# Performance work log

Hardware: AMD Instinct MI355X
Metric: run time of the kernel (lower is better)

The kernel has to match this reference:

```python
import jax, jax.numpy as jnp
import numpy as np

BN_EPS = 1e-3
SLOPE = 0.1
K = 100
CLUSTER_TEMP = 5.0


def setup_inputs() -> dict:
    key = jax.random.key(0)
    ks = jax.random.split(key, 5)
    N, Cin, Cout = 8192, 1, 64
    d = 49 * Cout  # (28/4)^2 * out_channels
    return {
        "x": jax.random.normal(ks[0], (N, Cin, 28, 28), jnp.float32),
        "conv1_w": jax.random.normal(ks[1], (128, Cin, 5, 5), jnp.float32) * 0.05,
        "conv1_b": jnp.zeros((128,), jnp.float32),
        "bn1_gamma": jnp.ones((128,), jnp.float32),
        "bn1_beta": jnp.zeros((128,), jnp.float32),
        "bn1_mean": jnp.zeros((128,), jnp.float32),
        "bn1_var": jnp.ones((128,), jnp.float32),
        "conv2_w": jax.random.normal(ks[2], (Cout, 128, 5, 5), jnp.float32) * 0.02,
        "conv2_b": jnp.zeros((Cout,), jnp.float32),
        "bn2_gamma": jnp.ones((Cout,), jnp.float32),
        "bn2_beta": jnp.zeros((Cout,), jnp.float32),
        "bn2_mean": jnp.zeros((Cout,), jnp.float32),
        "bn2_var": jnp.ones((Cout,), jnp.float32),
        "init_mu": jax.random.uniform(ks[3], (K, d), jnp.float32),
        "num_iter": 10,
    }


def _conv_bn_lrelu(x, w, b, gamma, beta, mean, var):
    # Conv2d(k=5, s=2, p=2) -> BatchNorm (eval/running stats) -> LeakyReLU(0.1)
    h = jax.lax.conv_general_dilated(
        x, w, window_strides=(2, 2), padding=[(2, 2), (2, 2)],
        dimension_numbers=("NCHW", "OIHW", "NCHW"))
    h = h + b[None, :, None, None]
    inv = gamma * jax.lax.rsqrt(var + BN_EPS)
    h = h * inv[None, :, None, None] + (beta - mean * inv)[None, :, None, None]
    return jnp.where(h >= 0, h, SLOPE * h)


def _cluster(data, mu, num_iter):
    # Row L2-normalize (equivalent to diag(1/||row||) @ data)
    data = data / jnp.linalg.norm(data, axis=1, keepdims=True)  # [n, d]
    for _ in range(num_iter):
        dist = data @ mu.T                                 # [n, K]
        r = jax.nn.softmax(CLUSTER_TEMP * dist, axis=1)    # [n, K]
        cluster_r = r.sum(axis=0)                          # [K]
        cluster_mean = r.T @ data                          # [K, d]
        mu = cluster_mean / cluster_r[:, None]
    dist = data @ mu.T
    r = jax.nn.softmax(CLUSTER_TEMP * dist, axis=1)
    return mu, r, dist


def reference(x, conv1_w, conv1_b, bn1_gamma, bn1_beta, bn1_mean, bn1_var,
              conv2_w, conv2_b, bn2_gamma, bn2_beta, bn2_mean, bn2_var,
              init_mu, num_iter):
    h = _conv_bn_lrelu(x, conv1_w, conv1_b, bn1_gamma, bn1_beta, bn1_mean, bn1_var)
    h = _conv_bn_lrelu(h, conv2_w, conv2_b, bn2_gamma, bn2_beta, bn2_mean, bn2_var)
    embeds = h.reshape(h.shape[0], -1)                     # [N, 49*Cout]
    mu_init, _, _ = _cluster(embeds, init_mu, int(num_iter))
    mu, r, dist = _cluster(embeds, jax.lax.stop_gradient(mu_init), 1)
    return mu, r, dist
```

## Files before the change

### kernel.cpp

```cpp
#include <hip/hip_runtime.h>
#include <hip/hip_bf16.h>
#include <math.h>

#define BN_EPS 1e-3f
#define SLOPE  0.1f
#define TEMP   5.0f
#define DDIM   3136

typedef __attribute__((ext_vector_type(8))) short bf16x8;
typedef __attribute__((ext_vector_type(4))) float f32x4;

static __device__ __forceinline__ short f2b(float f) {
  __hip_bfloat16 h = __float2bfloat16(f);
  return *reinterpret_cast<short*>(&h);
}

#define W2B_OFF   0u
#define W1B_OFF   102400u
#define DB_OFF    204800u
#define DB_SZ     (8192u*3136u/2u)
#define DT_OFF    (DB_OFF + DB_SZ)
#define DT_SZ     (8192u*3136u/2u)
#define MUB_OFF   (DT_OFF + DT_SZ)
#define MUB_SZ    (112u*3136u/2u)
#define MUF_OFF   (MUB_OFF + MUB_SZ)
#define MUF_SZ    (100u*3136u)
#define CMS_OFF   (MUF_OFF + MUF_SZ)
#define CMS_SZ    (16u*3136u*112u/2u)
#define RT_OFF    (CMS_OFF + CMS_SZ)
#define RT_SZ     (112u*8192u/2u)
#define CR_OFF    (RT_OFF + RT_SZ)

__global__ __launch_bounds__(256) void k_w2b(const float* __restrict__ w2,
                                             __hip_bfloat16* __restrict__ w2b) {
  int idx = blockIdx.x * 256 + threadIdx.x;
  if (idx >= 204800) return;
  int ci   = idx & 31;
  int lr   = (idx >> 5) & 15;
  int rest = idx >> 9;
  int kk   = rest % 100;
  int oct  = rest / 100;
  int oc   = oct * 16 + lr;
  int tap  = kk >> 2;
  int c    = ((kk & 3) << 5) + ci;
  w2b[idx] = __float2bfloat16(w2[(oc * 128 + c) * 25 + tap]);
}

__global__ __launch_bounds__(256) void k_w1b(const float* __restrict__ w1,
                                             __hip_bfloat16* __restrict__ w1b) {
  int idx = blockIdx.x * 256 + threadIdx.x;
  if (idx >= 4096) return;
  int k   = idx & 31;
  int lr  = (idx >> 5) & 15;
  int oct = idx >> 9;
  int oc  = oct * 16 + lr;
  float v = (k < 25) ? w1[oc * 25 + k] : 0.f;
  w1b[idx] = __float2bfloat16(v);
}

__global__ __launch_bounds__(256) void k_conv(
    const float* __restrict__ x,
    const __hip_bfloat16* __restrict__ w1bh, const float* __restrict__ b1,
    const float* __restrict__ g1,  const float* __restrict__ be1,
    const float* __restrict__ mn1, const float* __restrict__ vr1,
    const __hip_bfloat16* __restrict__ w2bh, const float* __restrict__ b2,
    const float* __restrict__ g2,  const float* __restrict__ be2,
    const float* __restrict__ mn2, const float* __restrict__ vr2,
    __hip_bfloat16* __restrict__ db) {
  __shared__ float xs[1024];
  __shared__ float bn2s[128];
  __shared__ float bn1a[128], bn1b[128];
  __shared__ float nrm[4];
  __shared__ __align__(16) __hip_bfloat16 h1s[197 * 128];

  const int t    = threadIdx.x;
  const int img  = blockIdx.x;
  const int lane = t & 63;
  const int wv   = t >> 6;
  const int lr   = lane & 15;
  const int kg   = lane >> 4;
  const short* w2b = (const short*)w2bh;
  const short* w1b = (const short*)w1bh;

  for (int i = t; i < 1024; i += 256) xs[i] = 0.f;
  if (t < 64) {
    float a2 = g2[t] * rsqrtf(vr2[t] + BN_EPS);
    bn2s[t]      = a2;
    bn2s[64 + t] = b2[t] * a2 + be2[t] - mn2[t] * a2;
    ((unsigned*)(h1s + 196 * 128))[t] = 0u;
  }
  if (t < 128) {
    float a1 = g1[t] * rsqrtf(vr1[t] + BN_EPS);
    bn1a[t] = a1;
    bn1b[t] = b1[t] * a1 + be1[t] - mn1[t] * a1;
  }
  __syncthreads();
  const float* xi = x + (size_t)img * 784;
  for (int i = t; i < 784; i += 256) {
    int yy = i / 28, xx = i % 28;
    xs[(yy + 2) * 32 + (xx + 2)] = xi[i];
  }
  __syncthreads();

  {
    bf16x8 a0 = *(const bf16x8*)(w1b + (2 * wv) * 512 + lr * 32 + kg * 8);
    bf16x8 a1 = *(const bf16x8*)(w1b + (2 * wv + 1) * 512 + lr * 32 + kg * 8);
    for (int pt = 0; pt < 13; ++pt) {
      const int px  = pt * 16 + lr;
      const int pxc = (px < 196) ? px : 195;
      const int oy  = pxc / 14, ox = pxc - 14 * (pxc / 14);
      const float* xb = xs + (2 * oy) * 32 + 2 * ox;
      short bs[8];
#pragma unroll
      for (int j = 0; j < 8; ++j) {
        int k   = kg * 8 + j;
        int tap = (k < 25) ? k : 0;
        int kh  = tap / 5, kw = tap - 5 * (tap / 5);
        bs[j] = f2b(xb[kh * 32 + kw]);
      }
      bf16x8 b;
#pragma unroll
      for (int j = 0; j < 8; ++j) b[j] = bs[j];
      f32x4 c0 = {0.f, 0.f, 0.f, 0.f}, c1 = {0.f, 0.f, 0.f, 0.f};
      c0 = __builtin_amdgcn_mfma_f32_16x16x32_bf16(a0, b, c0, 0, 0, 0);
      c1 = __builtin_amdgcn_mfma_f32_16x16x32_bf16(a1, b, c1, 0, 0, 0);
      if (px < 196) {
        const int swz = (px & 7) << 4;
        unsigned w0lo, w0hi, w1lo, w1hi;
        {
          float v[4], u[4];
#pragma unroll
          for (int r = 0; r < 4; ++r) {
            int oc = wv * 32 + kg * 4 + r;
            float h = c0[r] * bn1a[oc] + bn1b[oc];
            v[r] = (h >= 0.f) ? h : SLOPE * h;
            int oc2 = oc + 16;
            float h2 = c1[r] * bn1a[oc2] + bn1b[oc2];
            u[r] = (h2 >= 0.f) ? h2 : SLOPE * h2;
          }
          w0lo = (unsigned)(unsigned short)f2b(v[0]) |
                 ((unsigned)(unsigned short)f2b(v[1]) << 16);
          w0hi = (unsigned)(unsigned short)f2b(v[2]) |
                 ((unsigned)(unsigned short)f2b(v[3]) << 16);
          w1lo = (unsigned)(unsigned short)f2b(u[0]) |
                 ((unsigned)(unsigned short)f2b(u[1]) << 16);
          w1hi = (unsigned)(unsigned short)f2b(u[2]) |
                 ((unsigned)(unsigned short)f2b(u[3]) << 16);
        }
        char* base = (char*)h1s + px * 256;
        const int o0 = ((wv * 32 + kg * 4) * 2) ^ swz;
        const int o1 = ((wv * 32 + 16 + kg * 4) * 2) ^ swz;
        *(uint2*)(base + o0) = make_uint2(w0lo, w0hi);
        *(uint2*)(base + o1) = make_uint2(w1lo, w1hi);
      }
    }
  }
  __syncthreads();

  const int woff  = lr * 32 + kg * 8;
  const int kgoff = kg << 4;
  int pxA[4], oyA[4], oxA[4];
#pragma unroll
  for (int pt = 0; pt < 4; ++pt) {
    int p = pt * 16 + lr;
    pxA[pt] = p;
    oyA[pt] = p / 7;
    oxA[pt] = p - 7 * oyA[pt];
  }

  f32x4 acc[4][4];
#pragma unroll
  for (int oct = 0; oct < 4; ++oct)
#pragma unroll
    for (int pt = 0; pt < 4; ++pt) acc[oct][pt] = (f32x4){0.f, 0.f, 0.f, 0.f};

  const int s0 = 25 * wv, s1e = s0 + 25;
  int curtap = -1;
  int rowB[4], rowS[4];

  auto loadk = [&](int kk, bf16x8* areg, bf16x8* breg) {
    int tap = kk >> 2;
    if (tap != curtap) {
      curtap = tap;
      int kh = tap / 5, kw = tap - 5 * (tap / 5);
#pragma unroll
      for (int pt = 0; pt < 4; ++pt) {
        int iy = 2 * oyA[pt] - 2 + kh;
        int ix = 2 * oxA[pt] - 2 + kw;
        bool val = (pxA[pt] < 49) & ((unsigned)iy < 14u) & ((unsigned)ix < 14u);
        int ip = val ? iy * 14 + ix : 196;
        rowB[pt] = ip * 256;
        rowS[pt] = (ip & 7) << 4;
      }
    }
    int c01 = (kk & 3) << 6;
#pragma unroll
    for (int oct = 0; oct < 4; ++oct)
      areg[oct] = *(const bf16x8*)(w2b + ((oct * 100 + kk) << 9) + woff);
#pragma unroll
    for (int pt = 0; pt < 4; ++pt)
      breg[pt] = *(const bf16x8*)((const char*)h1s + rowB[pt] +
                                  ((c01 | kgoff) ^ rowS[pt]));
  };

  bf16x8 a[4], b[4], an[4], bn_[4];
  loadk(s0, a, b);
  for (int kk = s0; kk < s1e; ++kk) {
    if (kk + 1 < s1e) loadk(kk + 1, an, bn_);
#pragma unroll
    for (int oct = 0; oct < 4; ++oct)
#pragma unroll
      for (int pt = 0; pt < 4; ++pt)
        acc[oct][pt] = __builtin_amdgcn_mfma_f32_16x16x32_bf16(a[oct], b[pt],
                                                               acc[oct][pt], 0, 0, 0);
#pragma unroll
    for (int q = 0; q < 4; ++q) { a[q] = an[q]; b[q] = bn_[q]; }
  }
  __syncthreads();

  float* red = (float*)h1s;
  if (wv != 0) {
#pragma unroll
    for (int oct = 0; oct < 4; ++oct)
#pragma unroll
      for (int pt = 0; pt < 4; ++pt)
#pragma unroll
        for (int r = 0; r < 4; ++r)
          red[(wv - 1) * 4096 + ((oct * 4 + pt) * 4 + r) * 64 + lane] =
              acc[oct][pt][r];
  }
  __syncthreads();
  if (wv == 0) {
#pragma unroll
    for (int oct = 0; oct < 4; ++oct)
#pragma unroll
      for (int pt = 0; pt < 4; ++pt)
#pragma unroll
        for (int r = 0; r < 4; ++r) {
          const int i = (oct * 4 + pt) * 4 + r;
          float v = acc[oct][pt][r] + red[i * 64 + lane] +
                    red[4096 + i * 64 + lane] + red[8192 + i * 64 + lane];
          red[i * 64 + lane] = v;
        }
  }
  __syncthreads();

  float outv[16];
  float ss = 0.f;
#pragma unroll
  for (int pt = 0; pt < 4; ++pt) {
#pragma unroll
    for (int r = 0; r < 4; ++r) {
      const int i = ((wv * 4 + pt) * 4 + r);
      float v = red[i * 64 + lane];
      const int oc = wv * 16 + kg * 4 + r;
      v = v * bn2s[oc] + bn2s[64 + oc];
      v = (v >= 0.f) ? v : SLOPE * v;
      outv[pt * 4 + r] = v;
      if (pxA[pt] < 49) ss += v * v;
    }
  }
#pragma unroll
  for (int m = 1; m < 64; m <<= 1) ss += __shfl_xor(ss, m, 64);
  if (lane == 0) nrm[wv] = ss;
  __syncthreads();
  const float invn = rsqrtf(nrm[0] + nrm[1] + nrm[2] + nrm[3]);
  __hip_bfloat16* dro = db + (size_t)img * DDIM;
#pragma unroll
  for (int pt = 0; pt < 4; ++pt) {
    if (pxA[pt] < 49) {
#pragma unroll
      for (int r = 0; r < 4; ++r) {
        const int oc = wv * 16 + kg * 4 + r;
        dro[oc * 49 + pxA[pt]] = __float2bfloat16(outv[pt * 4 + r] * invn);
      }
    }
  }
}

__global__ __launch_bounds__(256) void k_tr(const __hip_bfloat16* __restrict__ dbh,
                                            __hip_bfloat16* __restrict__ dTh) {
  __shared__ short tile[64][72];
  const int t   = threadIdx.x;
  const int i   = t >> 2;
  const int seg = t & 3;
  const size_t img0 = (size_t)blockIdx.x * 64;
  const size_t d0   = (size_t)blockIdx.y * 64;
  const short* src = (const short*)dbh + (img0 + i) * DDIM + d0 + seg * 16;
  bf16x8 v0 = *(const bf16x8*)src;
  bf16x8 v1 = *(const bf16x8*)(src + 8);
  *(bf16x8*)&tile[i][seg * 16]     = v0;
  *(bf16x8*)&tile[i][seg * 16 + 8] = v1;
  __syncthreads();
  short tmp[16];
#pragma unroll
  for (int k = 0; k < 16; ++k) tmp[k] = tile[seg * 16 + k][i];
  short* dst = (short*)dTh + (d0 + i) * 8192 + img0 + seg * 16;
  *(bf16x8*)dst       = *(bf16x8*)tmp;
  *(bf16x8*)(dst + 8) = *((bf16x8*)tmp + 1);
}

__global__ __launch_bounds__(256) void k_muinit(const float* __restrict__ mu0,
                                                __hip_bfloat16* __restrict__ mub) {
  int idx = blockIdx.x * 256 + threadIdx.x;
  if (idx >= 112 * DDIM) return;
  int j = idx / DDIM, d = idx - j * DDIM;
  float v = (j < 100) ? mu0[j * DDIM + d] : 0.f;
  mub[idx] = __float2bfloat16(v);
}

__global__ __launch_bounds__(512) void k_dsm(
    const __hip_bfloat16* __restrict__ data,
    const __hip_bfloat16* __restrict__ mu,
    __hip_bfloat16* __restrict__ rT,
    float* __restrict__ cr,
    float* __restrict__ outr,
    float* __restrict__ outd,
    int final_flag) {
  __shared__ float red[7][64][29];
  const int t    = threadIdx.x;
  const int lane = t & 63;
  const int wv   = t >> 6;
  const int rowbase = blockIdx.x * 16;
  const int s0 = (98 * wv) >> 3;
  const int s1 = (98 * (wv + 1)) >> 3;
  const int lr = lane & 15;
  const int kg = lane >> 4;

  const __hip_bfloat16* arow = data + (size_t)(rowbase + lr) * DDIM + kg * 8;
  const __hip_bfloat16* brow = mu + (size_t)lr * DDIM + kg * 8;

  f32x4 acc[7];
#pragma unroll
  for (int i = 0; i < 7; ++i) acc[i] = (f32x4){0.f, 0.f, 0.f, 0.f};

  bf16x8 a, b[7], an, bn_[7];
  {
    const int k0 = s0 * 32;
    a = *(const bf16x8*)(arow + k0);
#pragma unroll
    for (int tl = 0; tl < 7; ++tl)
      b[tl] = *(const bf16x8*)(brow + (size_t)tl * 16 * DDIM + k0);
  }
  for (int s = s0; s < s1; ++s) {
    if (s + 1 < s1) {
      const int k1 = (s + 1) * 32;
      an = *(const bf16x8*)(arow + k1);
#pragma unroll
      for (int tl = 0; tl < 7; ++tl)
        bn_[tl] = *(const bf16x8*)(brow + (size_t)tl * 16 * DDIM + k1);
    }
#pragma unroll
    for (int tl = 0; tl < 7; ++tl)
      acc[tl] = __builtin_amdgcn_mfma_f32_16x16x32_bf16(a, b[tl], acc[tl], 0, 0, 0);
    a = an;
#pragma unroll
    for (int tl = 0; tl < 7; ++tl) b[tl] = bn_[tl];
  }

  if (wv != 0) {
#pragma unroll
    for (int tl = 0; tl < 7; ++tl)
#pragma unroll
      for (int r = 0; r < 4; ++r) red[wv - 1][lane][tl * 4 + r] = acc[tl][r];
  }
  __syncthreads();
  if (wv != 0) return;

#pragma unroll
  for (int tl = 0; tl < 7; ++tl)
#pragma unroll
    for (int r = 0; r < 4; ++r) {
      float v = acc[tl][r];
#pragma unroll
      for (int bk = 0; bk < 7; ++bk) v += red[bk][lane][tl * 4 + r];
      acc[tl][r] = v;
    }

  if (final_flag) {
#pragma unroll
    for (int tl = 0; tl < 7; ++tl) {
      const int col = tl * 16 + lr;
      if (col < 100) {
#pragma unroll
        for (int r = 0; r < 4; ++r)
          outd[(size_t)(rowbase + kg * 4 + r) * 100 + col] = acc[tl][r];
      }
    }
  }

#pragma unroll
  for (int r = 0; r < 4; ++r) {
    float m = -1e30f;
#pragma unroll
    for (int tl = 0; tl < 7; ++tl) {
      const bool valid = (tl < 6) || (lr < 4);
      m = fmaxf(m, valid ? acc[tl][r] : -1e30f);
    }
    m = fmaxf(m, __shfl_xor(m, 1, 64));
    m = fmaxf(m, __shfl_xor(m, 2, 64));
    m = fmaxf(m, __shfl_xor(m, 4, 64));
    m = fmaxf(m, __shfl_xor(m, 8, 64));
    float s = 0.f;
    float e[7];
#pragma unroll
    for (int tl = 0; tl < 7; ++tl) {
      const bool valid = (tl < 6) || (lr < 4);
      e[tl] = valid ? __expf(TEMP * (acc[tl][r] - m)) : 0.f;
      s += e[tl];
    }
    s += __shfl_xor(s, 1, 64);
    s += __shfl_xor(s, 2, 64);
    s += __shfl_xor(s, 4, 64);
    s += __shfl_xor(s, 8, 64);
    const float inv = 1.f / s;
#pragma unroll
    for (int tl = 0; tl < 7; ++tl) acc[tl][r] = e[tl] * inv;
  }

  if (final_flag) {
#pragma unroll
    for (int tl = 0; tl < 7; ++tl) {
      const int col = tl * 16 + lr;
      if (col < 100) {
#pragma unroll
        for (int r = 0; r < 4; ++r)
          outr[(size_t)(rowbase + kg * 4 + r) * 100 + col] = acc[tl][r];
      }
    }
    return;
  }

#pragma unroll
  for (int tl = 0; tl < 7; ++tl) {
    const int col = tl * 16 + lr;
    if (col < 100) {
#pragma unroll
      for (int r = 0; r < 4; ++r)
        rT[(size_t)col * 8192 + rowbase + kg * 4 + r] = __float2bfloat16(acc[tl][r]);
    }
  }
  float csum[7];
#pragma unroll
  for (int tl = 0; tl < 7; ++tl) {
    float cs = acc[tl][0] + acc[tl][1] + acc[tl][2] + acc[tl][3];
    cs += __shfl_xor(cs, 16, 64);
    cs += __shfl_xor(cs, 32, 64);
    csum[tl] = cs;
  }
  if (lane < 16) {
#pragma unroll
    for (int tl = 0; tl < 7; ++tl) {
      const int col = tl * 16 + lane;
      if (col < 100) atomicAdd(cr + col, csum[tl]);
    }
  }
}

__global__ __launch_bounds__(256) void k_mu(
    const __hip_bfloat16* __restrict__ dataT,
    const __hip_bfloat16* __restrict__ rT,
    __hip_bfloat16* __restrict__ cms) {
  const int t    = threadIdx.x;
  const int lane = t & 63;
  const int wv   = t >> 6;
  const int mbase = blockIdx.x * 64 + wv * 16;
  const int kbase = blockIdx.y * 512;
  const int lr = lane & 15;
  const int kg = lane >> 4;

  const __hip_bfloat16* arow = dataT + (size_t)(mbase + lr) * 8192 + kbase + kg * 8;
  const __hip_bfloat16* brow = rT + (size_t)lr * 8192 + kbase + kg * 8;

  f32x4 acc[7];
#pragma unroll
  for (int i = 0; i < 7; ++i) acc[i] = (f32x4){0.f, 0.f, 0.f, 0.f};

  bf16x8 a, b[7], an, bn_[7];
  a = *(const bf16x8*)(arow);
#pragma unroll
  for (int tl = 0; tl < 7; ++tl)
    b[tl] = *(const bf16x8*)(brow + (size_t)tl * 16 * 8192);
  for (int s = 0; s < 16; ++s) {
    if (s + 1 < 16) {
      const int k1 = (s + 1) * 32;
      an = *(const bf16x8*)(arow + k1);
#pragma unroll
      for (int tl = 0; tl < 7; ++tl)
        bn_[tl] = *(const bf16x8*)(brow + (size_t)tl * 16 * 8192 + k1);
    }
#pragma unroll
    for (int tl = 0; tl < 7; ++tl)
      acc[tl] = __builtin_amdgcn_mfma_f32_16x16x32_bf16(a, b[tl], acc[tl], 0, 0, 0);
    a = an;
#pragma unroll
    for (int tl = 0; tl < 7; ++tl) b[tl] = bn_[tl];
  }

  __hip_bfloat16* dst = cms + (size_t)blockIdx.y * (3136u * 112u);
#pragma unroll
  for (int tl = 0; tl < 7; ++tl) {
    const int col = tl * 16 + lr;
#pragma unroll
    for (int r = 0; r < 4; ++r)
      dst[(size_t)(mbase + kg * 4 + r) * 112 + col] = __float2bfloat16(acc[tl][r]);
  }
}

__global__ __launch_bounds__(256) void k_upd(const __hip_bfloat16* __restrict__ cms,
                                             const float* __restrict__ cr,
                                             float* __restrict__ muf,
                                             __hip_bfloat16* __restrict__ mub) {
  __shared__ float tile[64][113];
  const int t  = threadIdx.x;
  const int d0 = blockIdx.x * 64;
  for (int e = t; e < 64 * 112; e += 256) {
    int dd = e / 112, jj = e - dd * 112;
    const __hip_bfloat16* p = cms + (size_t)(d0 + dd) * 112 + jj;
    float v = 0.f;
#pragma unroll
    for (int s2 = 0; s2 < 16; ++s2)
      v += __bfloat162float(p[(size_t)s2 * (3136u * 112u)]);
    tile[dd][jj] = v;
  }
  __syncthreads();
  for (int e = t; e < 100 * 64; e += 256) {
    int jj = e >> 6, dd = e & 63;
    float v = tile[dd][jj] / cr[jj];
    muf[(size_t)jj * DDIM + d0 + dd] = v;
    mub[(size_t)jj * DDIM + d0 + dd] = __float2bfloat16(v);
  }
}

extern "C" void kernel_launch(void* const* d_in, const int* in_sizes, int n_in,
                              void* d_out, int out_size, void* d_ws, size_t ws_size,
                              hipStream_t stream) {
  const float* x   = (const float*)d_in[0];
  const float* w1  = (const float*)d_in[1];
  const float* b1  = (const float*)d_in[2];
  const float* g1  = (const float*)d_in[3];
  const float* be1 = (const float*)d_in[4];
  const float* mn1 = (const float*)d_in[5];
  const float* vr1 = (const float*)d_in[6];
  const float* w2  = (const float*)d_in[7];
  const float* b2  = (const float*)d_in[8];
  const float* g2  = (const float*)d_in[9];
  const float* be2 = (const float*)d_in[10];
  const float* mn2 = (const float*)d_in[11];
  const float* vr2 = (const float*)d_in[12];
  const float* mu0 = (const float*)d_in[13];

  float* ws = (float*)d_ws;
  __hip_bfloat16* w2b = (__hip_bfloat16*)(ws + W2B_OFF);
  __hip_bfloat16* w1b = (__hip_bfloat16*)(ws + W1B_OFF);
  __hip_bfloat16* db  = (__hip_bfloat16*)(ws + DB_OFF);
  __hip_bfloat16* dT  = (__hip_bfloat16*)(ws + DT_OFF);
  __hip_bfloat16* mub = (__hip_bfloat16*)(ws + MUB_OFF);
  float*          muf = ws + MUF_OFF;
  __hip_bfloat16* cms = (__hip_bfloat16*)(ws + CMS_OFF);
  __hip_bfloat16* rT  = (__hip_bfloat16*)(ws + RT_OFF);
  float*          cr  = ws + CR_OFF;
  float*          out = (float*)d_out;

  k_w2b<<<800, 256, 0, stream>>>(w2, w2b);
  k_w1b<<<16, 256, 0, stream>>>(w1, w1b);
  k_conv<<<8192, 256, 0, stream>>>(x, w1b, b1, g1, be1, mn1, vr1,
                                   w2b, b2, g2, be2, mn2, vr2, db);
  k_tr<<<dim3(128, 49), 256, 0, stream>>>(db, dT);
  k_muinit<<<(112 * DDIM + 255) / 256, 256, 0, stream>>>(mu0, mub);
  hipMemsetAsync(rT + (size_t)100 * 8192, 0, 12 * 8192 * sizeof(__hip_bfloat16),
                 stream);

  for (int it = 0; it < 11; ++it) {
    hipMemsetAsync(cr, 0, 128 * sizeof(float), stream);
    k_dsm<<<512, 512, 0, stream>>>(db, mub, rT, cr, nullptr, nullptr, 0);
    k_mu<<<dim3(49, 16), 256, 0, stream>>>(dT, rT, cms);
    k_upd<<<49, 256, 0, stream>>>(cms, cr, muf, mub);
  }

  k_dsm<<<512, 512, 0, stream>>>(db, mub, rT, cr, out + 313600, out + 1132800, 1);
  hipMemcpyAsync(out, muf, (size_t)MUF_SZ * sizeof(float),
                 hipMemcpyDeviceToDevice, stream);
}
```

Before: 1.850 ms.

## Retile cluster GEMMs: 32-row dsm blocks, 2x M-tile in k_mu, pre-zeroed cr buffers

k_dsm now handles 32 rows per block, using two row groups with a 4-way K split, and reduces partials through shared memory so all 8 waves share the softmax epilogue. k_mu computes two 16-row M tiles per wave so each loaded rT fragment feeds twice as many MFMAs, and dataT/cms are padded to 3200 rows to cover 25 blocks of 128. k_upd uses smaller 16-column tiles to spread work over more blocks. The per-iteration memset of cr is replaced by one upfront memset of 12 separate buffers. The cost is more register pressure in k_mu and fewer blocks for k_dsm and k_mu, which may lower occupancy.

```diff
diff --git a/kernel.cpp b/kernel.cpp
--- a/kernel.cpp
+++ b/kernel.cpp
@@ -6,6 +6,7 @@
 #define SLOPE  0.1f
 #define TEMP   5.0f
 #define DDIM   3136
+#define DDIMP  3200
 
 typedef __attribute__((ext_vector_type(8))) short bf16x8;
 typedef __attribute__((ext_vector_type(4))) float f32x4;
@@ -20,13 +21,13 @@
 #define DB_OFF    204800u
 #define DB_SZ     (8192u*3136u/2u)
 #define DT_OFF    (DB_OFF + DB_SZ)
-#define DT_SZ     (8192u*3136u/2u)
+#define DT_SZ     (3200u*8192u/2u)
 #define MUB_OFF   (DT_OFF + DT_SZ)
 #define MUB_SZ    (112u*3136u/2u)
 #define MUF_OFF   (MUB_OFF + MUB_SZ)
 #define MUF_SZ    (100u*3136u)
 #define CMS_OFF   (MUF_OFF + MUF_SZ)
-#define CMS_SZ    (16u*3136u*112u/2u)
+#define CMS_SZ    (16u*3200u*112u/2u)
 #define RT_OFF    (CMS_OFF + CMS_SZ)
 #define RT_SZ     (112u*8192u/2u)
 #define CR_OFF    (RT_OFF + RT_SZ)
@@ -317,17 +318,19 @@
     float* __restrict__ outr,
     float* __restrict__ outd,
     int final_flag) {
-  __shared__ float red[7][64][29];
+  __shared__ float red[8][64][29];
   const int t    = threadIdx.x;
   const int lane = t & 63;
   const int wv   = t >> 6;
-  const int rowbase = blockIdx.x * 16;
-  const int s0 = (98 * wv) >> 3;
-  const int s1 = (98 * (wv + 1)) >> 3;
+  const int rg   = wv >> 2;
+  const int ks   = wv & 3;
+  const int rowbase = blockIdx.x * 32;
+  const int s0 = (98 * ks) >> 2;
+  const int s1 = (98 * (ks + 1)) >> 2;
   const int lr = lane & 15;
   const int kg = lane >> 4;
 
-  const __hip_bfloat16* arow = data + (size_t)(rowbase + lr) * DDIM + kg * 8;
+  const __hip_bfloat16* arow = data + (size_t)(rowbase + rg * 16 + lr) * DDIM + kg * 8;
   const __hip_bfloat16* brow = mu + (size_t)lr * DDIM + kg * 8;
 
   f32x4 acc[7];
@@ -358,75 +361,65 @@
     for (int tl = 0; tl < 7; ++tl) b[tl] = bn_[tl];
   }
 
-  if (wv != 0) {
-#pragma unroll
-    for (int tl = 0; tl < 7; ++tl)
-#pragma unroll
-      for (int r = 0; r < 4; ++r) red[wv - 1][lane][tl * 4 + r] = acc[tl][r];
-  }
-  __syncthreads();
-  if (wv != 0) return;
-
 #pragma unroll
   for (int tl = 0; tl < 7; ++tl)
 #pragma unroll
-    for (int r = 0; r < 4; ++r) {
-      float v = acc[tl][r];
-#pragma unroll
-      for (int bk = 0; bk < 7; ++bk) v += red[bk][lane][tl * 4 + r];
-      acc[tl][r] = v;
-    }
+    for (int r = 0; r < 4; ++r) red[wv][lane][tl * 4 + r] = acc[tl][r];
+  __syncthreads();
+
+  const int r_   = lane >> 4;
+  const int kg_t = wv & 3;
+  const int rg_t = wv >> 2;
+  const int grow = rowbase + 4 * wv + r_;
+  float v[7];
+#pragma unroll
+  for (int tl = 0; tl < 7; ++tl) {
+    float s = 0.f;
+#pragma unroll
+    for (int k2 = 0; k2 < 4; ++k2)
+      s += red[rg_t * 4 + k2][kg_t * 16 + lr][tl * 4 + r_];
+    v[tl] = s;
+  }
 
   if (final_flag) {
 #pragma unroll
     for (int tl = 0; tl < 7; ++tl) {
       const int col = tl * 16 + lr;
-      if (col < 100) {
-#pragma unroll
-        for (int r = 0; r < 4; ++r)
-          outd[(size_t)(rowbase + kg * 4 + r) * 100 + col] = acc[tl][r];
-      }
-    }
-  }
-
-#pragma unroll
-  for (int r = 0; r < 4; ++r) {
-    float m = -1e30f;
-#pragma unroll
-    for (int tl = 0; tl < 7; ++tl) {
-      const bool valid = (tl < 6) || (lr < 4);
-      m = fmaxf(m, valid ? acc[tl][r] : -1e30f);
-    }
-    m = fmaxf(m, __shfl_xor(m, 1, 64));
-    m = fmaxf(m, __shfl_xor(m, 2, 64));
-    m = fmaxf(m, __shfl_xor(m, 4, 64));
-    m = fmaxf(m, __shfl_xor(m, 8, 64));
-    float s = 0.f;
-    float e[7];
-#pragma unroll
-    for (int tl = 0; tl < 7; ++tl) {
-      const bool valid = (tl < 6) || (lr < 4);
-      e[tl] = valid ? __expf(TEMP * (acc[tl][r] - m)) : 0.f;
-      s += e[tl];
-    }
-    s += __shfl_xor(s, 1, 64);
-    s += __shfl_xor(s, 2, 64);
-    s += __shfl_xor(s, 4, 64);
-    s += __shfl_xor(s, 8, 64);
-    const float inv = 1.f / s;
-#pragma unroll
-    for (int tl = 0; tl < 7; ++tl) acc[tl][r] = e[tl] * inv;
-  }
+      if (col < 100) outd[(size_t)grow * 100 + col] = v[tl];
+    }
+  }
+
+  float m = -1e30f;
+#pragma unroll
+  for (int tl = 0; tl < 7; ++tl) {
+    const bool valid = (tl < 6) || (lr < 4);
+    m = fmaxf(m, valid ? v[tl] : -1e30f);
+  }
+  m = fmaxf(m, __shfl_xor(m, 1, 64));
+  m = fmaxf(m, __shfl_xor(m, 2, 64));
+  m = fmaxf(m, __shfl_xor(m, 4, 64));
+  m = fmaxf(m, __shfl_xor(m, 8, 64));
+  float e[7];
+  float s = 0.f;
+#pragma unroll
+  for (int tl = 0; tl < 7; ++tl) {
+    const bool valid = (tl < 6) || (lr < 4);
+    e[tl] = valid ? __expf(TEMP * (v[tl] - m)) : 0.f;
+    s += e[tl];
+  }
+  s += __shfl_xor(s, 1, 64);
+  s += __shfl_xor(s, 2, 64);
+  s += __shfl_xor(s, 4, 64);
+  s += __shfl_xor(s, 8, 64);
+  const float inv = 1.f / s;
+#pragma unroll
+  for (int tl = 0; tl < 7; ++tl) e[tl] *= inv;
 
   if (final_flag) {
 #pragma unroll
     for (int tl = 0; tl < 7; ++tl) {
       const int col = tl * 16 + lr;
-      if (col < 100) {
-#pragma unroll
-        for (int r = 0; r < 4; ++r)
-          outr[(size_t)(rowbase + kg * 4 + r) * 100 + col] = acc[tl][r];
-      }
+      if (col < 100) outr[(size_t)grow * 100 + col] = e[tl];
     }
     return;
   }
@@ -434,25 +427,22 @@
 #pragma unroll
   for (int tl = 0; tl < 7; ++tl) {
     const int col = tl * 16 + lr;
-    if (col < 100) {
-#pragma unroll
-      for (int r = 0; r < 4; ++r)
-        rT[(size_t)col * 8192 + rowbase + kg * 4 + r] = __float2bfloat16(acc[tl][r]);
-    }
-  }
-  float csum[7];
+    if (col < 100)
+      rT[(size_t)col * 8192 + grow] = __float2bfloat16(e[tl]);
+  }
+  float cs[7];
 #pragma unroll
   for (int tl = 0; tl < 7; ++tl) {
-    float cs = acc[tl][0] + acc[tl][1] + acc[tl][2] + acc[tl][3];
-    cs += __shfl_xor(cs, 16, 64);
-    cs += __shfl_xor(cs, 32, 64);
-    csum[tl] = cs;
+    float c2 = e[tl];
+    c2 += __shfl_xor(c2, 16, 64);
+    c2 += __shfl_xor(c2, 32, 64);
+    cs[tl] = c2;
   }
   if (lane < 16) {
 #pragma unroll
     for (int tl = 0; tl < 7; ++tl) {
       const int col = tl * 16 + lane;
-      if (col < 100) atomicAdd(cr + col, csum[tl]);
+      if (col < 100) atomicAdd(cr + col, cs[tl]);
     }
   }
 }
@@ -464,46 +454,57 @@
   const int t    = threadIdx.x;
   const int lane = t & 63;
   const int wv   = t >> 6;
-  const int mbase = blockIdx.x * 64 + wv * 16;
+  const int mbase = blockIdx.x * 128 + wv * 32;
   const int kbase = blockIdx.y * 512;
   const int lr = lane & 15;
   const int kg = lane >> 4;
 
-  const __hip_bfloat16* arow = dataT + (size_t)(mbase + lr) * 8192 + kbase + kg * 8;
-  const __hip_bfloat16* brow = rT + (size_t)lr * 8192 + kbase + kg * 8;
-
-  f32x4 acc[7];
-#pragma unroll
-  for (int i = 0; i < 7; ++i) acc[i] = (f32x4){0.f, 0.f, 0.f, 0.f};
-
-  bf16x8 a, b[7], an, bn_[7];
-  a = *(const bf16x8*)(arow);
+  const __hip_bfloat16* arow0 = dataT + (size_t)(mbase + lr) * 8192 + kbase + kg * 8;
+  const __hip_bfloat16* arow1 = arow0 + (size_t)16 * 8192;
+  const __hip_bfloat16* brow  = rT + (size_t)lr * 8192 + kbase + kg * 8;
+
+  f32x4 acc[2][7];
+#pragma unroll
+  for (int mt = 0; mt < 2; ++mt)
+#pragma unroll
+    for (int i = 0; i < 7; ++i) acc[mt][i] = (f32x4){0.f, 0.f, 0.f, 0.f};
+
+  bf16x8 a0, a1, b[7], a0n, a1n, bn_[7];
+  a0 = *(const bf16x8*)(arow0);
+  a1 = *(const bf16x8*)(arow1);
 #pragma unroll
   for (int tl = 0; tl < 7; ++tl)
     b[tl] = *(const bf16x8*)(brow + (size_t)tl * 16 * 8192);
   for (int s = 0; s < 16; ++s) {
     if (s + 1 < 16) {
       const int k1 = (s + 1) * 32;
-      an = *(const bf16x8*)(arow + k1);
+      a0n = *(const bf16x8*)(arow0 + k1);
+      a1n = *(const bf16x8*)(arow1 + k1);
 #pragma unroll
       for (int tl = 0; tl < 7; ++tl)
         bn_[tl] = *(const bf16x8*)(brow + (size_t)tl * 16 * 8192 + k1);
     }
 #pragma unroll
-    for (int tl = 0; tl < 7; ++tl)
-      acc[tl] = __builtin_amdgcn_mfma_f32_16x16x32_bf16(a, b[tl], acc[tl], 0, 0, 0);
-    a = an;
+    for (int tl = 0; tl < 7; ++tl) {
+      acc[0][tl] = __builtin_amdgcn_mfma_f32_16x16x32_bf16(a0, b[tl], acc[0][tl], 0, 0, 0);
+      acc[1][tl] = __builtin_amdgcn_mfma_f32_16x16x32_bf16(a1, b[tl], acc[1][tl], 0, 0, 0);
+    }
+    a0 = a0n; a1 = a1n;
 #pragma unroll
     for (int tl = 0; tl < 7; ++tl) b[tl] = bn_[tl];
   }
 
-  __hip_bfloat16* dst = cms + (size_t)blockIdx.y * (3136u * 112u);
-#pragma unroll
-  for (int tl = 0; tl < 7; ++tl) {
-    const int col = tl * 16 + lr;
-#pragma unroll
-    for (int r = 0; r < 4; ++r)
-      dst[(size_t)(mbase + kg * 4 + r) * 112 + col] = __float2bfloat16(acc[tl][r]);
+  __hip_bfloat16* dst = cms + (size_t)blockIdx.y * (3200u * 112u);
+#pragma unroll
+  for (int mt = 0; mt < 2; ++mt) {
+#pragma unroll
+    for (int tl = 0; tl < 7; ++tl) {
+      const int col = tl * 16 + lr;
+#pragma unroll
+      for (int r = 0; r < 4; ++r)
+        dst[(size_t)(mbase + mt * 16 + kg * 4 + r) * 112 + col] =
+            __float2bfloat16(acc[mt][tl][r]);
+    }
   }
 }
 
@@ -511,21 +512,21 @@
                                              const float* __restrict__ cr,
                                              float* __restrict__ muf,
                                              __hip_bfloat16* __restrict__ mub) {
-  __shared__ float tile[64][113];
+  __shared__ float tile[16][113];
   const int t  = threadIdx.x;
-  const int d0 = blockIdx.x * 64;
-  for (int e = t; e < 64 * 112; e += 256) {
+  const int d0 = blockIdx.x * 16;
+  for (int e = t; e < 16 * 112; e += 256) {
     int dd = e / 112, jj = e - dd * 112;
     const __hip_bfloat16* p = cms + (size_t)(d0 + dd) * 112 + jj;
     float v = 0.f;
 #pragma unroll
     for (int s2 = 0; s2 < 16; ++s2)
-      v += __bfloat162float(p[(size_t)s2 * (3136u * 112u)]);
+      v += __bfloat162float(p[(size_t)s2 * (3200u * 112u)]);
     tile[dd][jj] = v;
   }
   __syncthreads();
-  for (int e = t; e < 100 * 64; e += 256) {
-    int jj = e >> 6, dd = e & 63;
+  for (int e = t; e < 100 * 16; e += 256) {
+    int jj = e >> 4, dd = e & 15;
     float v = tile[dd][jj] / cr[jj];
     muf[(size_t)jj * DDIM + d0 + dd] = v;
     mub[(size_t)jj * DDIM + d0 + dd] = __float2bfloat16(v);
@@ -559,7 +560,7 @@
   float*          muf = ws + MUF_OFF;
   __hip_bfloat16* cms = (__hip_bfloat16*)(ws + CMS_OFF);
   __hip_bfloat16* rT  = (__hip_bfloat16*)(ws + RT_OFF);
-  float*          cr  = ws + CR_OFF;
+  float*          crb = ws + CR_OFF;
   float*          out = (float*)d_out;
 
   k_w2b<<<800, 256, 0, stream>>>(w2, w2b);
@@ -570,15 +571,17 @@
   k_muinit<<<(112 * DDIM + 255) / 256, 256, 0, stream>>>(mu0, mub);
   hipMemsetAsync(rT + (size_t)100 * 8192, 0, 12 * 8192 * sizeof(__hip_bfloat16),
                  stream);
+  hipMemsetAsync(crb, 0, 12 * 128 * sizeof(float), stream);
 
   for (int it = 0; it < 11; ++it) {
-    hipMemsetAsync(cr, 0, 128 * sizeof(float), stream);
-    k_dsm<<<512, 512, 0, stream>>>(db, mub, rT, cr, nullptr, nullptr, 0);
-    k_mu<<<dim3(49, 16), 256, 0, stream>>>(dT, rT, cms);
-    k_upd<<<49, 256, 0, stream>>>(cms, cr, muf, mub);
-  }
-
-  k_dsm<<<512, 512, 0, stream>>>(db, mub, rT, cr, out + 313600, out + 1132800, 1);
+    float* cr = crb + it * 128;
+    k_dsm<<<256, 512, 0, stream>>>(db, mub, rT, cr, nullptr, nullptr, 0);
+    k_mu<<<dim3(25, 16), 256, 0, stream>>>(dT, rT, cms);
+    k_upd<<<196, 256, 0, stream>>>(cms, cr, muf, mub);
+  }
+
+  k_dsm<<<256, 512, 0, stream>>>(db, mub, rT, crb + 11 * 128,
+                                 out + 313600, out + 1132800, 1);
   hipMemcpyAsync(out, muf, (size_t)MUF_SZ * sizeof(float),
                  hipMemcpyDeviceToDevice, stream);
 }
```

Result: slower. 1.932 ms (+4.4%).

## Fuse cluster-mean update into distance and mu kernels via atomics and double-buffered sums

Applied to the files above, without the earlier changes.

The separate k_upd reduction kernel is removed. k_mu now atomically accumulates fp32 unnormalized cluster sums into a ping-pong buffer and zeroes the other one, and k_dsm reads those fp32 sums, converts them to bf16 on the fly and scales by 1/cluster_r after its reduction. k_mu gets a taller M tile (two 16-row tiles per wave) for more reuse. Smaller changes: the weight-prep kernels are merged, per-launch memsets are dropped, conv BN constants move into registers, the input is stored as bf16 in LDS, and the LDS swizzle is altered. The trade-offs are heavy fp32 atomic traffic, fp32 mu reads in k_dsm that are no longer software-prefetched, and atomic ordering that makes results nondeterministic.

```diff
diff --git a/kernel.cpp b/kernel.cpp
--- a/kernel.cpp
+++ b/kernel.cpp
@@ -17,45 +17,43 @@
 
 #define W2B_OFF   0u
 #define W1B_OFF   102400u
-#define DB_OFF    204800u
+#define DB_OFF    104448u
 #define DB_SZ     (8192u*3136u/2u)
 #define DT_OFF    (DB_OFF + DB_SZ)
-#define DT_SZ     (8192u*3136u/2u)
-#define MUB_OFF   (DT_OFF + DT_SZ)
-#define MUB_SZ    (112u*3136u/2u)
-#define MUF_OFF   (MUB_OFF + MUB_SZ)
-#define MUF_SZ    (100u*3136u)
-#define CMS_OFF   (MUF_OFF + MUF_SZ)
-#define CMS_SZ    (16u*3136u*112u/2u)
-#define RT_OFF    (CMS_OFF + CMS_SZ)
+#define DT_SZ     (3200u*8192u/2u)
+#define CMA_OFF   (DT_OFF + DT_SZ)
+#define CM_SZ     (112u*3136u)
+#define CMB_OFF   (CMA_OFF + CM_SZ)
+#define RT_OFF    (CMB_OFF + CM_SZ)
 #define RT_SZ     (112u*8192u/2u)
-#define CR_OFF    (RT_OFF + RT_SZ)
-
-__global__ __launch_bounds__(256) void k_w2b(const float* __restrict__ w2,
-                                             __hip_bfloat16* __restrict__ w2b) {
+#define CRB_OFF   (RT_OFF + RT_SZ)
+
+__global__ __launch_bounds__(256) void k_wprep(const float* __restrict__ w2,
+                                               const float* __restrict__ w1,
+                                               __hip_bfloat16* __restrict__ w2b,
+                                               __hip_bfloat16* __restrict__ w1b) {
   int idx = blockIdx.x * 256 + threadIdx.x;
-  if (idx >= 204800) return;
-  int ci   = idx & 31;
-  int lr   = (idx >> 5) & 15;
-  int rest = idx >> 9;
-  int kk   = rest % 100;
-  int oct  = rest / 100;
-  int oc   = oct * 16 + lr;
-  int tap  = kk >> 2;
-  int c    = ((kk & 3) << 5) + ci;
-  w2b[idx] = __float2bfloat16(w2[(oc * 128 + c) * 25 + tap]);
-}
-
-__global__ __launch_bounds__(256) void k_w1b(const float* __restrict__ w1,
-                                             __hip_bfloat16* __restrict__ w1b) {
-  int idx = blockIdx.x * 256 + threadIdx.x;
-  if (idx >= 4096) return;
-  int k   = idx & 31;
-  int lr  = (idx >> 5) & 15;
-  int oct = idx >> 9;
-  int oc  = oct * 16 + lr;
-  float v = (k < 25) ? w1[oc * 25 + k] : 0.f;
-  w1b[idx] = __float2bfloat16(v);
+  if (idx < 204800) {
+    int ci   = idx & 31;
+    int lr   = (idx >> 5) & 15;
+    int rest = idx >> 9;
+    int kk   = rest % 100;
+    int oct  = rest / 100;
+    int oc   = oct * 16 + lr;
+    int tap  = kk >> 2;
+    int c    = ((kk & 3) << 5) + ci;
+    w2b[idx] = __float2bfloat16(w2[(oc * 128 + c) * 25 + tap]);
+  } else {
+    int j = idx - 204800;
+    if (j < 4096) {
+      int k   = j & 31;
+      int lr  = (j >> 5) & 15;
+      int oct = j >> 9;
+      int oc  = oct * 16 + lr;
+      float v = (k < 25) ? w1[oc * 25 + k] : 0.f;
+      w1b[j] = __float2bfloat16(v);
+    }
+  }
 }
 
 __global__ __launch_bounds__(256) void k_conv(
@@ -67,9 +65,7 @@
     const float* __restrict__ g2,  const float* __restrict__ be2,
     const float* __restrict__ mn2, const float* __restrict__ vr2,
     __hip_bfloat16* __restrict__ db) {
-  __shared__ float xs[1024];
-  __shared__ float bn2s[128];
-  __shared__ float bn1a[128], bn1b[128];
+  __shared__ unsigned short xsb[1024];
   __shared__ float nrm[4];
   __shared__ __align__(16) __hip_bfloat16 h1s[197 * 128];
 
@@ -82,23 +78,31 @@
   const short* w2b = (const short*)w2bh;
   const short* w1b = (const short*)w1bh;
 
-  for (int i = t; i < 1024; i += 256) xs[i] = 0.f;
-  if (t < 64) {
-    float a2 = g2[t] * rsqrtf(vr2[t] + BN_EPS);
-    bn2s[t]      = a2;
-    bn2s[64 + t] = b2[t] * a2 + be2[t] - mn2[t] * a2;
-    ((unsigned*)(h1s + 196 * 128))[t] = 0u;
-  }
-  if (t < 128) {
-    float a1 = g1[t] * rsqrtf(vr1[t] + BN_EPS);
-    bn1a[t] = a1;
-    bn1b[t] = b1[t] * a1 + be1[t] - mn1[t] * a1;
-  }
+  float a1v[8], s1v[8];
+#pragma unroll
+  for (int r = 0; r < 4; ++r) {
+    int oc = wv * 32 + kg * 4 + r;
+    float a = g1[oc] * rsqrtf(vr1[oc] + BN_EPS);
+    a1v[r] = a; s1v[r] = b1[oc] * a + be1[oc] - mn1[oc] * a;
+    int oc2 = oc + 16;
+    float a2_ = g1[oc2] * rsqrtf(vr1[oc2] + BN_EPS);
+    a1v[4 + r] = a2_; s1v[4 + r] = b1[oc2] * a2_ + be1[oc2] - mn1[oc2] * a2_;
+  }
+  float a2v[4], s2v[4];
+#pragma unroll
+  for (int r = 0; r < 4; ++r) {
+    int oc = wv * 16 + kg * 4 + r;
+    float a = g2[oc] * rsqrtf(vr2[oc] + BN_EPS);
+    a2v[r] = a; s2v[r] = b2[oc] * a + be2[oc] - mn2[oc] * a;
+  }
+
+  for (int i = t; i < 1024; i += 256) xsb[i] = 0;
+  if (t < 64) ((unsigned*)(h1s + 196 * 128))[t] = 0u;
   __syncthreads();
   const float* xi = x + (size_t)img * 784;
   for (int i = t; i < 784; i += 256) {
     int yy = i / 28, xx = i % 28;
-    xs[(yy + 2) * 32 + (xx + 2)] = xi[i];
+    xsb[(yy + 2) * 32 + (xx + 2)] = (unsigned short)f2b(xi[i]);
   }
   __syncthreads();
 
@@ -109,14 +113,14 @@
       const int px  = pt * 16 + lr;
       const int pxc = (px < 196) ? px : 195;
       const int oy  = pxc / 14, ox = pxc - 14 * (pxc / 14);
-      const float* xb = xs + (2 * oy) * 32 + 2 * ox;
+      const unsigned short* xb = xsb + (2 * oy) * 32 + 2 * ox;
       short bs[8];
 #pragma unroll
       for (int j = 0; j < 8; ++j) {
         int k   = kg * 8 + j;
         int tap = (k < 25) ? k : 0;
         int kh  = tap / 5, kw = tap - 5 * (tap / 5);
-        bs[j] = f2b(xb[kh * 32 + kw]);
+        bs[j] = (short)xb[kh * 32 + kw];
       }
       bf16x8 b;
 #pragma unroll
@@ -125,28 +129,23 @@
       c0 = __builtin_amdgcn_mfma_f32_16x16x32_bf16(a0, b, c0, 0, 0, 0);
       c1 = __builtin_amdgcn_mfma_f32_16x16x32_bf16(a1, b, c1, 0, 0, 0);
       if (px < 196) {
-        const int swz = (px & 7) << 4;
-        unsigned w0lo, w0hi, w1lo, w1hi;
-        {
-          float v[4], u[4];
-#pragma unroll
-          for (int r = 0; r < 4; ++r) {
-            int oc = wv * 32 + kg * 4 + r;
-            float h = c0[r] * bn1a[oc] + bn1b[oc];
-            v[r] = (h >= 0.f) ? h : SLOPE * h;
-            int oc2 = oc + 16;
-            float h2 = c1[r] * bn1a[oc2] + bn1b[oc2];
-            u[r] = (h2 >= 0.f) ? h2 : SLOPE * h2;
-          }
-          w0lo = (unsigned)(unsigned short)f2b(v[0]) |
-                 ((unsigned)(unsigned short)f2b(v[1]) << 16);
-          w0hi = (unsigned)(unsigned short)f2b(v[2]) |
-                 ((unsigned)(unsigned short)f2b(v[3]) << 16);
-          w1lo = (unsigned)(unsigned short)f2b(u[0]) |
-                 ((unsigned)(unsigned short)f2b(u[1]) << 16);
-          w1hi = (unsigned)(unsigned short)f2b(u[2]) |
-                 ((unsigned)(unsigned short)f2b(u[3]) << 16);
+        const int swz = ((px >> 1) & 7) << 4;
+        float v[4], u[4];
+#pragma unroll
+        for (int r = 0; r < 4; ++r) {
+          float h = c0[r] * a1v[r] + s1v[r];
+          v[r] = (h >= 0.f) ? h : SLOPE * h;
+          float h2 = c1[r] * a1v[4 + r] + s1v[4 + r];
+          u[r] = (h2 >= 0.f) ? h2 : SLOPE * h2;
         }
+        unsigned w0lo = (unsigned)(unsigned short)f2b(v[0]) |
+                        ((unsigned)(unsigned short)f2b(v[1]) << 16);
+        unsigned w0hi = (unsigned)(unsigned short)f2b(v[2]) |
+                        ((unsigned)(unsigned short)f2b(v[3]) << 16);
+        unsigned w1lo = (unsigned)(unsigned short)f2b(u[0]) |
+                        ((unsigned)(unsigned short)f2b(u[1]) << 16);
+        unsigned w1hi = (unsigned)(unsigned short)f2b(u[2]) |
+                        ((unsigned)(unsigned short)f2b(u[3]) << 16);
         char* base = (char*)h1s + px * 256;
         const int o0 = ((wv * 32 + kg * 4) * 2) ^ swz;
         const int o1 = ((wv * 32 + 16 + kg * 4) * 2) ^ swz;
@@ -190,7 +189,7 @@
         bool val = (pxA[pt] < 49) & ((unsigned)iy < 14u) & ((unsigned)ix < 14u);
         int ip = val ? iy * 14 + ix : 196;
         rowB[pt] = ip * 256;
-        rowS[pt] = (ip & 7) << 4;
+        rowS[pt] = ((ip >> 1) & 7) << 4;
       }
     }
     int c01 = (kk & 3) << 6;
@@ -253,8 +252,7 @@
     for (int r = 0; r < 4; ++r) {
       const int i = ((wv * 4 + pt) * 4 + r);
       float v = red[i * 64 + lane];
-      const int oc = wv * 16 + kg * 4 + r;
-      v = v * bn2s[oc] + bn2s[64 + oc];
+      v = v * a2v[r] + s2v[r];
       v = (v >= 0.f) ? v : SLOPE * v;
       outv[pt * 4 + r] = v;
       if (pxA[pt] < 49) ss += v * v;
@@ -300,20 +298,28 @@
   *(bf16x8*)(dst + 8) = *((bf16x8*)tmp + 1);
 }
 
-__global__ __launch_bounds__(256) void k_muinit(const float* __restrict__ mu0,
-                                                __hip_bfloat16* __restrict__ mub) {
+__global__ __launch_bounds__(256) void k_init(const float* __restrict__ mu0,
+                                              float* __restrict__ cmA,
+                                              float* __restrict__ cmB,
+                                              __hip_bfloat16* __restrict__ rT,
+                                              float* __restrict__ crb) {
   int idx = blockIdx.x * 256 + threadIdx.x;
-  if (idx >= 112 * DDIM) return;
-  int j = idx / DDIM, d = idx - j * DDIM;
-  float v = (j < 100) ? mu0[j * DDIM + d] : 0.f;
-  mub[idx] = __float2bfloat16(v);
+  if (idx < (int)CM_SZ) {
+    int j = idx / DDIM;
+    cmA[idx] = (j < 100) ? mu0[idx] : 0.f;
+    cmB[idx] = 0.f;
+  }
+  if (idx < 12 * 8192)
+    rT[(size_t)100 * 8192 + idx] = __float2bfloat16(0.f);
+  if (idx < 12 * 128) crb[idx] = (idx < 128) ? 1.f : 0.f;
 }
 
 __global__ __launch_bounds__(512) void k_dsm(
     const __hip_bfloat16* __restrict__ data,
-    const __hip_bfloat16* __restrict__ mu,
+    const float* __restrict__ cm,
+    const float* __restrict__ crv,
     __hip_bfloat16* __restrict__ rT,
-    float* __restrict__ cr,
+    float* __restrict__ crnext,
     float* __restrict__ outr,
     float* __restrict__ outd,
     int final_flag) {
@@ -328,34 +334,25 @@
   const int kg = lane >> 4;
 
   const __hip_bfloat16* arow = data + (size_t)(rowbase + lr) * DDIM + kg * 8;
-  const __hip_bfloat16* brow = mu + (size_t)lr * DDIM + kg * 8;
+  const float* brow = cm + (size_t)lr * DDIM + kg * 8;
 
   f32x4 acc[7];
 #pragma unroll
   for (int i = 0; i < 7; ++i) acc[i] = (f32x4){0.f, 0.f, 0.f, 0.f};
 
-  bf16x8 a, b[7], an, bn_[7];
-  {
-    const int k0 = s0 * 32;
-    a = *(const bf16x8*)(arow + k0);
-#pragma unroll
-    for (int tl = 0; tl < 7; ++tl)
-      b[tl] = *(const bf16x8*)(brow + (size_t)tl * 16 * DDIM + k0);
-  }
   for (int s = s0; s < s1; ++s) {
-    if (s + 1 < s1) {
-      const int k1 = (s + 1) * 32;
-      an = *(const bf16x8*)(arow + k1);
-#pragma unroll
-      for (int tl = 0; tl < 7; ++tl)
-        bn_[tl] = *(const bf16x8*)(brow + (size_t)tl * 16 * DDIM + k1);
-    }
-#pragma unroll
-    for (int tl = 0; tl < 7; ++tl)
-      acc[tl] = __builtin_amdgcn_mfma_f32_16x16x32_bf16(a, b[tl], acc[tl], 0, 0, 0);
-    a = an;
-#pragma unroll
-    for (int tl = 0; tl < 7; ++tl) b[tl] = bn_[tl];
+    const int k0 = s * 32;
+    bf16x8 a = *(const bf16x8*)(arow + k0);
+#pragma unroll
+    for (int tl = 0; tl < 7; ++tl) {
+      const float* bp = brow + (size_t)tl * 16 * DDIM + k0;
+      float4 f0 = *(const float4*)(bp);
+      float4 f1 = *(const float4*)(bp + 4);
+      bf16x8 b;
+      b[0] = f2b(f0.x); b[1] = f2b(f0.y); b[2] = f2b(f0.z); b[3] = f2b(f0.w);
+      b[4] = f2b(f1.x); b[5] = f2b(f1.y); b[6] = f2b(f1.z); b[7] = f2b(f1.w);
+      acc[tl] = __builtin_amdgcn_mfma_f32_16x16x32_bf16(a, b, acc[tl], 0, 0, 0);
+    }
   }
 
   if (wv != 0) {
@@ -376,6 +373,14 @@
       for (int bk = 0; bk < 7; ++bk) v += red[bk][lane][tl * 4 + r];
       acc[tl][r] = v;
     }
+
+#pragma unroll
+  for (int tl = 0; tl < 7; ++tl) {
+    const int col = tl * 16 + lr;
+    const float cinv = (col < 100) ? 1.f / crv[col] : 0.f;
+#pragma unroll
+    for (int r = 0; r < 4; ++r) acc[tl][r] *= cinv;
+  }
 
   if (final_flag) {
 #pragma unroll
@@ -452,7 +457,7 @@
 #pragma unroll
     for (int tl = 0; tl < 7; ++tl) {
       const int col = tl * 16 + lane;
-      if (col < 100) atomicAdd(cr + col, csum[tl]);
+      if (col < 100) atomicAdd(crnext + col, csum[tl]);
     }
   }
 }
@@ -460,76 +465,80 @@
 __global__ __launch_bounds__(256) void k_mu(
     const __hip_bfloat16* __restrict__ dataT,
     const __hip_bfloat16* __restrict__ rT,
-    __hip_bfloat16* __restrict__ cms) {
+    float* __restrict__ cmnext,
+    float* __restrict__ cmzero) {
   const int t    = threadIdx.x;
   const int lane = t & 63;
   const int wv   = t >> 6;
-  const int mbase = blockIdx.x * 64 + wv * 16;
+  const int mbase = blockIdx.x * 128 + wv * 32;
   const int kbase = blockIdx.y * 512;
   const int lr = lane & 15;
   const int kg = lane >> 4;
 
-  const __hip_bfloat16* arow = dataT + (size_t)(mbase + lr) * 8192 + kbase + kg * 8;
-  const __hip_bfloat16* brow = rT + (size_t)lr * 8192 + kbase + kg * 8;
-
-  f32x4 acc[7];
-#pragma unroll
-  for (int i = 0; i < 7; ++i) acc[i] = (f32x4){0.f, 0.f, 0.f, 0.f};
-
-  bf16x8 a, b[7], an, bn_[7];
-  a = *(const bf16x8*)(arow);
+  const __hip_bfloat16* arow0 = dataT + (size_t)(mbase + lr) * 8192 + kbase + kg * 8;
+  const __hip_bfloat16* arow1 = arow0 + (size_t)16 * 8192;
+  const __hip_bfloat16* brow  = rT + (size_t)lr * 8192 + kbase + kg * 8;
+
+  f32x4 acc[2][7];
+#pragma unroll
+  for (int mt = 0; mt < 2; ++mt)
+#pragma unroll
+    for (int i = 0; i < 7; ++i) acc[mt][i] = (f32x4){0.f, 0.f, 0.f, 0.f};
+
+  bf16x8 a0, a1, b[7], a0n, a1n, bn_[7];
+  a0 = *(const bf16x8*)(arow0);
+  a1 = *(const bf16x8*)(arow1);
 #pragma unroll
   for (int tl = 0; tl < 7; ++tl)
     b[tl] = *(const bf16x8*)(brow + (size_t)tl * 16 * 8192);
   for (int s = 0; s < 16; ++s) {
     if (s + 1 < 16) {
       const int k1 = (s + 1) * 32;
-      an = *(const bf16x8*)(arow + k1);
+      a0n = *(const bf16x8*)(arow0 + k1);
+      a1n = *(const bf16x8*)(arow1 + k1);
 #pragma unroll
       for (int tl = 0; tl < 7; ++tl)
         bn_[tl] = *(const bf16x8*)(brow + (size_t)tl * 16 * 8192 + k1);
     }
 #pragma unroll
-    for (int tl = 0; tl < 7; ++tl)
-      acc[tl] = __builtin_amdgcn_mfma_f32_16x16x32_bf16(a, b[tl], acc[tl], 0, 0, 0);
-    a = an;
+    for (int tl = 0; tl < 7; ++tl) {
+      acc[0][tl] = __builtin_amdgcn_mfma_f32_16x16x32_bf16(a0, b[tl], acc[0][tl], 0, 0, 0);
+      acc[1][tl] = __builtin_amdgcn_mfma_f32_16x16x32_bf16(a1, b[tl], acc[1][tl], 0, 0, 0);
+    }
+    a0 = a0n; a1 = a1n;
 #pragma unroll
     for (int tl = 0; tl < 7; ++tl) b[tl] = bn_[tl];
   }
 
-  __hip_bfloat16* dst = cms + (size_t)blockIdx.y * (3136u * 112u);
-#pragma unroll
-  for (int tl = 0; tl < 7; ++tl) {
-    const int col = tl * 16 + lr;
-#pragma unroll
-    for (int r = 0; r < 4; ++r)
-      dst[(size_t)(mbase + kg * 4 + r) * 112 + col] = __float2bfloat16(acc[tl][r]);
-  }
-}
-
-__global__ __launch_bounds__(256) void k_upd(const __hip_bfloat16* __restrict__ cms,
-                                             const float* __restrict__ cr,
-                                             float* __restrict__ muf,
-                                             __hip_bfloat16* __restrict__ mub) {
-  __shared__ float tile[64][113];
-  const int t  = threadIdx.x;
-  const int d0 = blockIdx.x * 64;
-  for (int e = t; e < 64 * 112; e += 256) {
-    int dd = e / 112, jj = e - dd * 112;
-    const __hip_bfloat16* p = cms + (size_t)(d0 + dd) * 112 + jj;
-    float v = 0.f;
-#pragma unroll
-    for (int s2 = 0; s2 < 16; ++s2)
-      v += __bfloat162float(p[(size_t)s2 * (3136u * 112u)]);
-    tile[dd][jj] = v;
-  }
-  __syncthreads();
-  for (int e = t; e < 100 * 64; e += 256) {
-    int jj = e >> 6, dd = e & 63;
-    float v = tile[dd][jj] / cr[jj];
-    muf[(size_t)jj * DDIM + d0 + dd] = v;
-    mub[(size_t)jj * DDIM + d0 + dd] = __float2bfloat16(v);
-  }
+#pragma unroll
+  for (int mt = 0; mt < 2; ++mt) {
+#pragma unroll
+    for (int tl = 0; tl < 7; ++tl) {
+      const int col = tl * 16 + lr;
+#pragma unroll
+      for (int r = 0; r < 4; ++r) {
+        const int d = mbase + mt * 16 + kg * 4 + r;
+        if (d < DDIM)
+          atomicAdd(cmnext + (size_t)col * DDIM + d, acc[mt][tl][r]);
+      }
+    }
+  }
+
+  const int bid  = blockIdx.y * 25 + blockIdx.x;
+  const int base = bid * 880;
+  for (int i = t; i < 880; i += 256) {
+    int idx = base + i;
+    if (idx < (int)CM_SZ) cmzero[idx] = 0.f;
+  }
+}
+
+__global__ __launch_bounds__(256) void k_mufin(const float* __restrict__ cm,
+                                               const float* __restrict__ crv,
+                                               float* __restrict__ outmu) {
+  int idx = blockIdx.x * 256 + threadIdx.x;
+  if (idx >= 100 * DDIM) return;
+  int j = idx / DDIM;
+  outmu[idx] = cm[idx] / crv[j];
 }
 
 extern "C" void kernel_launch(void* const* d_in, const int* in_sizes, int n_in,
@@ -555,30 +564,28 @@
   __hip_bfloat16* w1b = (__hip_bfloat16*)(ws + W1B_OFF);
   __hip_bfloat16* db  = (__hip_bfloat16*)(ws + DB_OFF);
   __hip_bfloat16* dT  = (__hip_bfloat16*)(ws + DT_OFF);
-  __hip_bfloat16* mub = (__hip_bfloat16*)(ws + MUB_OFF);
-  float*          muf = ws + MUF_OFF;
-  __hip_bfloat16* cms = (__hip_bfloat16*)(ws + CMS_OFF);
+  float*          cmA = ws + CMA_OFF;
+  float*          cmB = ws + CMB_OFF;
   __hip_bfloat16* rT  = (__hip_bfloat16*)(ws + RT_OFF);
-  float*          cr  = ws + CR_OFF;
+  float*          crb = ws + CRB_OFF;
   float*          out = (float*)d_out;
 
-  k_w2b<<<800, 256, 0, stream>>>(w2, w2b);
-  k_w1b<<<16, 256, 0, stream>>>(w1, w1b);
+  k_wprep<<<816, 256, 0, stream>>>(w2, w1, w2b, w1b);
   k_conv<<<8192, 256, 0, stream>>>(x, w1b, b1, g1, be1, mn1, vr1,
                                    w2b, b2, g2, be2, mn2, vr2, db);
   k_tr<<<dim3(128, 49), 256, 0, stream>>>(db, dT);
-  k_muinit<<<(112 * DDIM + 255) / 256, 256, 0, stream>>>(mu0, mub);
-  hipMemsetAsync(rT + (size_t)100 * 8192, 0, 12 * 8192 * sizeof(__hip_bfloat16),
-                 stream);
-
+  k_init<<<(CM_SZ + 255) / 256, 256, 0, stream>>>(mu0, cmA, cmB, rT, crb);
+
+  float* cms[2] = {cmA, cmB};
   for (int it = 0; it < 11; ++it) {
-    hipMemsetAsync(cr, 0, 128 * sizeof(float), stream);
-    k_dsm<<<512, 512, 0, stream>>>(db, mub, rT, cr, nullptr, nullptr, 0);
-    k_mu<<<dim3(49, 16), 256, 0, stream>>>(dT, rT, cms);
-    k_upd<<<49, 256, 0, stream>>>(cms, cr, muf, mub);
-  }
-
-  k_dsm<<<512, 512, 0, stream>>>(db, mub, rT, cr, out + 313600, out + 1132800, 1);
-  hipMemcpyAsync(out, muf, (size_t)MUF_SZ * sizeof(float),
-                 hipMemcpyDeviceToDevice, stream);
-}
+    float* cur = cms[it & 1];
+    float* nxt = cms[(it + 1) & 1];
+    k_dsm<<<512, 512, 0, stream>>>(db, cur, crb + it * 128, rT,
+                                   crb + (it + 1) * 128, nullptr, nullptr, 0);
+    k_mu<<<dim3(25, 16), 256, 0, stream>>>(dT, rT, nxt, cur);
+  }
+
+  k_dsm<<<512, 512, 0, stream>>>(db, cms[1], crb + 11 * 128, rT, crb,
+                                 out + 313600, out + 1132800, 1);
+  k_mufin<<<(100 * DDIM + 255) / 256, 256, 0, stream>>>(cms[1], crb + 11 * 128, out);
+}
```

Result: slower. 2.547 ms (+37.7%).
